# Kernel tuning notes

Measured on AMD Instinct MI355X. Metric: run time of the kernel, lower is better.

The kernel has to match this reference:

```python
import jax, jax.numpy as jnp
import numpy as np

DIM = 1024
ATT_DIM = 1024
NUM_HEADS = 16
HEAD_DIM = ATT_DIM // NUM_HEADS


def setup_inputs() -> dict:
    key = jax.random.key(0)
    ks = jax.random.split(key, 13)
    s = lambda fan_in: 1.0 / np.sqrt(fan_in)
    bsz, n = 8, 1024
    x = jax.random.normal(ks[0], (bsz, n, DIM), dtype=jnp.float32)
    # Linear weights stored as [in, out] (apply via x @ W + b)
    Wq = jax.random.uniform(ks[1], (DIM, ATT_DIM), minval=-s(DIM), maxval=s(DIM))
    bq = jax.random.uniform(ks[2], (ATT_DIM,), minval=-s(DIM), maxval=s(DIM))
    Wk = jax.random.uniform(ks[3], (DIM, ATT_DIM), minval=-s(DIM), maxval=s(DIM))
    bk = jax.random.uniform(ks[4], (ATT_DIM,), minval=-s(DIM), maxval=s(DIM))
    Wv = jax.random.uniform(ks[5], (DIM, ATT_DIM), minval=-s(DIM), maxval=s(DIM))
    bv = jax.random.uniform(ks[6], (ATT_DIM,), minval=-s(DIM), maxval=s(DIM))
    Win = jax.random.uniform(ks[7], (DIM, HEAD_DIM), minval=-s(DIM), maxval=s(DIM))
    bin_ = jax.random.uniform(ks[8], (HEAD_DIM,), minval=-s(DIM), maxval=s(DIM))
    d_in1 = HEAD_DIM * (NUM_HEADS + 1)
    W1 = jax.random.uniform(ks[9], (d_in1, 2 * DIM), minval=-s(d_in1), maxval=s(d_in1))
    b1 = jax.random.uniform(ks[10], (2 * DIM,), minval=-s(d_in1), maxval=s(d_in1))
    W2 = jax.random.uniform(ks[11], (2 * DIM, DIM), minval=-s(2 * DIM), maxval=s(2 * DIM))
    b2 = jax.random.uniform(ks[12], (DIM,), minval=-s(2 * DIM), maxval=s(2 * DIM))
    return {"x": x, "Wq": Wq, "bq": bq, "Wk": Wk, "bk": bk, "Wv": Wv, "bv": bv,
            "Win": Win, "bin_": bin_, "W1": W1, "b1": b1, "W2": W2, "b2": b2}


def reference(x, Wq, bq, Wk, bk, Wv, bv, Win, bin_, W1, b1, W2, b2):
    bsz, n, _ = x.shape
    scaling = HEAD_DIM ** (-0.5)
    # [b, n, h, d]
    q = (x @ Wq + bq).reshape(bsz, n, NUM_HEADS, HEAD_DIM) * scaling
    k = (x @ Wk + bk).reshape(bsz, n, NUM_HEADS, HEAD_DIM)
    v = (x @ Wv + bv).reshape(bsz, n, NUM_HEADS, HEAD_DIM)
    # scores [b, h, n, n]
    score = jnp.einsum('bihd,bjhd->bhij', q, k)
    diag = jnp.eye(n, dtype=bool)  # self positions masked with -inf
    score = jnp.where(diag[None, None], -jnp.inf, score)
    attn = jax.nn.softmax(score, axis=-1)
    out = jnp.einsum('bhij,bjhd->bihd', attn, v).reshape(bsz, n, NUM_HEADS * HEAD_DIM)
    in_ = (x @ Win + bin_)  # [b, n, head_dim]
    out = jnp.concatenate([out, in_], axis=-1)
    h = jax.nn.relu(out @ W1 + b1)
    return h @ W2 + b2
```

## Files before the change

kernel.cpp:

```cpp
#include <hip/hip_runtime.h>

typedef __bf16 bf16;
typedef __attribute__((ext_vector_type(8))) __bf16 bf16x8;
typedef __attribute__((ext_vector_type(4))) __bf16 bf16x4;
typedef __attribute__((ext_vector_type(4))) short short4_t;
typedef __attribute__((ext_vector_type(4))) float floatx4;

typedef const void __attribute__((address_space(1)))* gas1p;
typedef void __attribute__((address_space(3)))* las3p;

#define LOG2E 1.44269504088896340736f

static constexpr int D_MODEL = 1024;
static constexpr int N_HEADS = 16;
static constexpr int HDIM    = 64;
static constexpr int BSZ     = 8;
static constexpr int SEQ     = 1024;
static constexpr int ROWS    = BSZ * SEQ;
static constexpr int FF_IN   = 1088;
static constexpr int FF_HID  = 2048;
static constexpr int QKV_LD  = 3072;

__device__ __forceinline__ floatx4 mfma_bf16(bf16x8 a, bf16x8 b, floatx4 c) {
  return __builtin_amdgcn_mfma_f32_16x16x32_bf16(a, b, c, 0, 0, 0);
}

__device__ __forceinline__ floatx4 mfma16(bf16x4 a, bf16x4 b, floatx4 c) {
#if __has_builtin(__builtin_amdgcn_mfma_f32_16x16x16_bf16)
  return __builtin_amdgcn_mfma_f32_16x16x16_bf16(a, b, c, 0, 0, 0);
#else
  return __builtin_amdgcn_mfma_f32_16x16x16bf16_1k(
      __builtin_bit_cast(short4_t, a), __builtin_bit_cast(short4_t, b), c, 0, 0, 0);
#endif
}

__device__ __forceinline__ float flex_load(const void* src, size_t idx, int isbf) {
  return isbf ? (float)((const bf16*)src)[idx] : ((const float*)src)[idx];
}

__global__ void detect_kernel(const unsigned* __restrict__ w, int* __restrict__ flag) {
  __shared__ int cnt;
  if (threadIdx.x == 0) cnt = 0;
  __syncthreads();
  int hits = 0;
  for (int i = threadIdx.x; i < 4096; i += 256) {
    const unsigned v = w[(size_t)i * 997 + 13];
    const unsigned b = (v >> 8) & 0x7F;
    hits += (b >= 0x3B && b <= 0x41) ? 1 : 0;
  }
  atomicAdd(&cnt, hits);
  __syncthreads();
  if (threadIdx.x == 0) *flag = (cnt > 2048) ? 1 : 0;
}

__global__ __launch_bounds__(256)
void x_to_bf16_kernel(const void* __restrict__ src, bf16* __restrict__ dst,
                      const int* __restrict__ flag) {
  const int isbf = *flag;
  const size_t i = ((size_t)blockIdx.x * 256 + threadIdx.x) * 8;
  bf16x8 o;
  if (isbf) {
    o = *reinterpret_cast<const bf16x8*>((const bf16*)src + i);
  } else {
    const float4 f0 = *reinterpret_cast<const float4*>((const float*)src + i);
    const float4 f1 = *reinterpret_cast<const float4*>((const float*)src + i + 4);
    o[0] = (bf16)f0.x; o[1] = (bf16)f0.y; o[2] = (bf16)f0.z; o[3] = (bf16)f0.w;
    o[4] = (bf16)f1.x; o[5] = (bf16)f1.y; o[6] = (bf16)f1.z; o[7] = (bf16)f1.w;
  }
  *reinterpret_cast<bf16x8*>(dst + i) = o;
}

__global__ __launch_bounds__(256)
void bias_all_kernel(const void* bq, const void* bk, const void* bv,
                     const void* bin, const void* b1, const void* b2,
                     float* __restrict__ dst, const int* __restrict__ flag) {
  const int isbf = *flag;
  const int i = blockIdx.x * 256 + threadIdx.x;
  if (i < 1024)      dst[i] = flex_load(bq, i, isbf) * 0.125f;
  else if (i < 2048) dst[i] = flex_load(bk, i - 1024, isbf);
  else if (i < 3072) dst[i] = flex_load(bv, i - 2048, isbf);
  else if (i < 3136) dst[i] = flex_load(bin, i - 3072, isbf);
  else if (i < 5184) dst[i] = flex_load(b1, i - 3136, isbf);
  else if (i < 6208) dst[i] = flex_load(b2, i - 5184, isbf);
}

struct TransJobs {
  const void* src[6];
  bf16* dst[6];
  int R[6], C[6];
  int tiles_x[6];
  int tile_base[7];
  float scale[6];
};

__global__ __launch_bounds__(256)
void transpose_all_kernel(TransJobs J, const int* __restrict__ flag) {
  __shared__ float tile[32][33];
  const int isbf = *flag;
  const int bid = blockIdx.x;
  int j = 0;
#pragma unroll
  for (int t = 1; t < 6; t++) j += (bid >= J.tile_base[t]) ? 1 : 0;
  const int t = bid - J.tile_base[j];
  const int c0 = (t % J.tiles_x[j]) * 32, r0 = (t / J.tiles_x[j]) * 32;
  const void* src = J.src[j];
  bf16* dst = J.dst[j];
  const int R = J.R[j], C = J.C[j];
  const float scale = J.scale[j];
  const int tx = threadIdx.x & 31, ty = threadIdx.x >> 5;
  for (int i = ty; i < 32; i += 8)
    tile[i][tx] = flex_load(src, (size_t)(r0 + i) * C + (c0 + tx), isbf);
  __syncthreads();
  for (int i = ty; i < 32; i += 8)
    dst[(size_t)(c0 + i) * R + (r0 + tx)] = (bf16)(tile[tx][i] * scale);
}

__global__ __launch_bounds__(256)
void transpose_v_kernel(const bf16* __restrict__ v, bf16* __restrict__ vt) {
  __shared__ float tile[32][33];
  const int bh = blockIdx.z, b = bh >> 4, h = bh & 15;
  const int s0 = blockIdx.x * 32, d0 = blockIdx.y * 32;
  const int tx = threadIdx.x & 31, ty = threadIdx.x >> 5;
  const bf16* src = v + (size_t)b * SEQ * QKV_LD + 2048 + h * HDIM;
  bf16* dst = vt + (size_t)bh * HDIM * SEQ;
  for (int i = ty; i < 32; i += 8)
    tile[i][tx] = (float)src[(size_t)(s0 + i) * QKV_LD + d0 + tx];
  __syncthreads();
  for (int i = ty; i < 32; i += 8)
    dst[(size_t)(d0 + i) * SEQ + s0 + tx] = (bf16)tile[tx][i];
}

template <int BN, bool DO_RELU, bool OUT_FLEX>
__global__ __launch_bounds__(256)
void gemm_bt(const bf16* __restrict__ A, const bf16* __restrict__ BT,
             const float* __restrict__ bias,
             void* __restrict__ Cv, int N, int K, int ldc,
             bf16* __restrict__ C2, int ldc2, int nsplit, int nvalid,
             const int* __restrict__ flag) {
  constexpr int BM = 128, BK = 64;
  constexpr int TCN = BN / 32;
  constexpr int ACH = (BM * BK) / (256 * 8);
  constexpr int BCH = (BN * BK) / (256 * 8);
  __shared__ bf16 As[BM * BK];
  __shared__ bf16 Bs[BN * BK];
  const int tid = threadIdx.x;
  const int wave = tid >> 6, lane = tid & 63;
  const int quad = lane >> 4, lo = lane & 15;
  const int wm = wave >> 1, wn = wave & 1;
  const int m0 = blockIdx.x * BM;
  const int n0 = blockIdx.y * BN;

  floatx4 acc[4][TCN];
#pragma unroll
  for (int i = 0; i < 4; i++)
#pragma unroll
    for (int j = 0; j < TCN; j++) acc[i][j] = floatx4{0.f, 0.f, 0.f, 0.f};

  for (int kb = 0; kb < K; kb += BK) {
#pragma unroll
    for (int u = 0; u < ACH; u++) {
      const int c = u * 256 + tid;
      const int row = c >> 3, col = c & 7;
      const int gcol = col ^ (row & 7);
      const bf16* g = A + (size_t)(m0 + row) * K + kb + gcol * 8;
      __builtin_amdgcn_global_load_lds((gas1p)g, (las3p)(As + c * 8), 16, 0, 0);
    }
#pragma unroll
    for (int u = 0; u < BCH; u++) {
      const int c = u * 256 + tid;
      const int row = c >> 3, col = c & 7;
      const int gcol = col ^ (row & 7);
      const bf16* g = BT + (size_t)(n0 + row) * K + kb + gcol * 8;
      __builtin_amdgcn_global_load_lds((gas1p)g, (las3p)(Bs + c * 8), 16, 0, 0);
    }
    __syncthreads();
#pragma unroll
    for (int kk = 0; kk < 2; kk++) {
      bf16x8 af[4], bfr[TCN];
#pragma unroll
      for (int tr = 0; tr < 4; tr++) {
        const int row = wm * 64 + tr * 16 + lo;
        const int cc = (kk * 4 + quad) ^ (lo & 7);
        af[tr] = *reinterpret_cast<const bf16x8*>(As + row * BK + cc * 8);
      }
#pragma unroll
      for (int tc = 0; tc < TCN; tc++) {
        const int row = wn * (BN / 2) + tc * 16 + lo;
        const int cc = (kk * 4 + quad) ^ (lo & 7);
        bfr[tc] = *reinterpret_cast<const bf16x8*>(Bs + row * BK + cc * 8);
      }
#pragma unroll
      for (int tr = 0; tr < 4; tr++)
#pragma unroll
        for (int tc = 0; tc < TCN; tc++)
          acc[tr][tc] = mfma_bf16(af[tr], bfr[tc], acc[tr][tc]);
    }
    __syncthreads();
  }

  const int isbf = OUT_FLEX ? *flag : 1;
#pragma unroll
  for (int tc = 0; tc < TCN; tc++) {
    const int col = n0 + wn * (BN / 2) + tc * 16 + lo;
    const float bval = bias[col];
    if (col < nsplit) {
#pragma unroll
      for (int tr = 0; tr < 4; tr++) {
        const int rbase = m0 + wm * 64 + tr * 16 + quad * 4;
#pragma unroll
        for (int r = 0; r < 4; r++) {
          float v = acc[tr][tc][r] + bval;
          if (DO_RELU) v = fmaxf(v, 0.f);
          const size_t idx = (size_t)(rbase + r) * ldc + col;
          if (!OUT_FLEX || isbf) ((bf16*)Cv)[idx] = (bf16)v;
          else                   ((float*)Cv)[idx] = v;
        }
      }
    } else if (col < nvalid) {
#pragma unroll
      for (int tr = 0; tr < 4; tr++) {
        const int rbase = m0 + wm * 64 + tr * 16 + quad * 4;
#pragma unroll
        for (int r = 0; r < 4; r++) {
          float v = acc[tr][tc][r] + bval;
          if (DO_RELU) v = fmaxf(v, 0.f);
          C2[(size_t)(rbase + r) * ldc2 + (col - nsplit)] = (bf16)v;
        }
      }
    }
  }
}

__global__ __launch_bounds__(256)
void attn_kernel(const bf16* __restrict__ QKV, const bf16* __restrict__ Vt,
                 bf16* __restrict__ Cc) {
  __shared__ bf16 Ks[64 * 64];
  __shared__ bf16 Vs[64 * 64];
  const int bid = blockIdx.x;
  const int xcd = bid & 7, g = bid >> 3;
  const int ib = g & 7, bh = (g >> 3) * 8 + xcd;
  const int b = bh >> 4, h = bh & 15;
  const int i0 = ib * 128;
  const int tid = threadIdx.x, wave = tid >> 6, lane = tid & 63;
  const int quad = lane >> 4, lo = lane & 15;
  const int iw = i0 + wave * 32;
  const bf16* qptr = QKV + (size_t)b * SEQ * QKV_LD + h * HDIM;
  const bf16* kptr = QKV + (size_t)b * SEQ * QKV_LD + 1024 + h * HDIM;
  const bf16* vptr = Vt + (size_t)bh * HDIM * SEQ;

  bf16x8 qf[2][2];
#pragma unroll
  for (int it = 0; it < 2; it++)
#pragma unroll
    for (int kf = 0; kf < 2; kf++)
      qf[it][kf] = *reinterpret_cast<const bf16x8*>(
          qptr + (size_t)(iw + it * 16 + lo) * QKV_LD + kf * 32 + quad * 8);

  floatx4 oacc[2][4];
  float lrow[2] = {0.f, 0.f};
#pragma unroll
  for (int it = 0; it < 2; it++)
#pragma unroll
    for (int dt = 0; dt < 4; dt++) oacc[it][dt] = floatx4{0.f, 0.f, 0.f, 0.f};

  for (int jb = 0; jb < SEQ / 64; jb++) {
    const int j0 = jb * 64;
#pragma unroll
    for (int u = 0; u < 2; u++) {
      const int c = u * 256 + tid;
      const int row = c >> 3, col = c & 7;
      const int gcol = col ^ (row & 7);
      __builtin_amdgcn_global_load_lds(
          (gas1p)(kptr + (size_t)(j0 + row) * QKV_LD + gcol * 8),
          (las3p)(Ks + c * 8), 16, 0, 0);
      __builtin_amdgcn_global_load_lds(
          (gas1p)(vptr + (size_t)row * SEQ + j0 + gcol * 8),
          (las3p)(Vs + c * 8), 16, 0, 0);
    }
    __syncthreads();

    floatx4 sacc[2][4];
#pragma unroll
    for (int it = 0; it < 2; it++)
#pragma unroll
      for (int mt = 0; mt < 4; mt++) sacc[it][mt] = floatx4{0.f, 0.f, 0.f, 0.f};
#pragma unroll
    for (int mt = 0; mt < 4; mt++) {
      const int r = mt * 16 + lo;
      const int cc0 = quad ^ (lo & 7);
      const int cc1 = (4 + quad) ^ (lo & 7);
      const bf16x8 k0 = *reinterpret_cast<const bf16x8*>(Ks + r * 64 + cc0 * 8);
      const bf16x8 k1 = *reinterpret_cast<const bf16x8*>(Ks + r * 64 + cc1 * 8);
#pragma unroll
      for (int it = 0; it < 2; it++) {
        sacc[it][mt] = mfma_bf16(k0, qf[it][0], sacc[it][mt]);
        sacc[it][mt] = mfma_bf16(k1, qf[it][1], sacc[it][mt]);
      }
    }

    if (j0 == (iw & ~63)) {
#pragma unroll
      for (int it = 0; it < 2; it++) {
        const int ig = iw + it * 16 + lo;
#pragma unroll
        for (int mt = 0; mt < 4; mt++)
#pragma unroll
          for (int r = 0; r < 4; r++)
            if (j0 + mt * 16 + quad * 4 + r == ig) sacc[it][mt][r] = -1e30f;
      }
    }

    bf16x4 pfrag[2][4];
#pragma unroll
    for (int it = 0; it < 2; it++) {
      float s = 0.f;
#pragma unroll
      for (int mt = 0; mt < 4; mt++) {
        bf16x4 pk;
#pragma unroll
        for (int r = 0; r < 4; r++) {
          const float p = exp2f(sacc[it][mt][r] * LOG2E);
          s += p;
          pk[r] = (bf16)p;
        }
        pfrag[it][mt] = pk;
      }
      s += __shfl_xor(s, 16);
      s += __shfl_xor(s, 32);
      lrow[it] += s;
    }

#pragma unroll
    for (int dt = 0; dt < 4; dt++) {
      const int r = dt * 16 + lo;
#pragma unroll
      for (int kt = 0; kt < 4; kt++) {
        const int gch = kt * 2 + (quad >> 1);
        const int cc = gch ^ (lo & 7);
        const bf16x4 vf = *reinterpret_cast<const bf16x4*>(
            Vs + r * 64 + cc * 8 + (quad & 1) * 4);
#pragma unroll
        for (int it = 0; it < 2; it++)
          oacc[it][dt] = mfma16(vf, pfrag[it][kt], oacc[it][dt]);
      }
    }
    __syncthreads();
  }

#pragma unroll
  for (int it = 0; it < 2; it++) {
    const int ig = iw + it * 16 + lo;
    const float inv = 1.0f / lrow[it];
    bf16* cb = Cc + ((size_t)b * SEQ + ig) * FF_IN + h * HDIM;
#pragma unroll
    for (int dt = 0; dt < 4; dt++) {
      bf16x4 o;
#pragma unroll
      for (int r = 0; r < 4; r++) o[r] = (bf16)(oacc[it][dt][r] * inv);
      *reinterpret_cast<bf16x4*>(cb + dt * 16 + quad * 4) = o;
    }
  }
}

extern "C" void kernel_launch(void* const* d_in, const int* in_sizes, int n_in,
                              void* d_out, int out_size, void* d_ws, size_t ws_size,
                              hipStream_t stream) {
  (void)in_sizes; (void)n_in; (void)out_size; (void)ws_size;
  const void* x   = d_in[0];
  const void* Wq  = d_in[1];
  const void* bq  = d_in[2];
  const void* Wk  = d_in[3];
  const void* bk  = d_in[4];
  const void* Wv  = d_in[5];
  const void* bv  = d_in[6];
  const void* Win = d_in[7];
  const void* bin = d_in[8];
  const void* W1  = d_in[9];
  const void* b1  = d_in[10];
  const void* W2  = d_in[11];
  const void* b2  = d_in[12];

  size_t off = 0;
  char* wsb = (char*)d_ws;
  auto alloc = [&](size_t bytes) {
    void* p = (void*)(wsb + off);
    off += (bytes + 255) & ~(size_t)255;
    return p;
  };
  int*   flag  = (int*)alloc(4);
  bf16*  xbf   = (bf16*)alloc((size_t)ROWS * D_MODEL * 2);
  bf16*  WqkvT = (bf16*)alloc((size_t)3200 * 1024 * 2);
  bf16*  W1T   = (bf16*)alloc((size_t)FF_HID * FF_IN * 2);
  bf16*  W2T   = (bf16*)alloc((size_t)D_MODEL * FF_HID * 2);
  float* biasf = (float*)alloc(6208 * 4);
  bf16*  qkv   = (bf16*)alloc((size_t)ROWS * QKV_LD * 2);
  bf16*  vtb   = (bf16*)alloc((size_t)ROWS * D_MODEL * 2);
  bf16*  cbuf  = (bf16*)alloc((size_t)ROWS * FF_IN * 2);
  bf16*  hbuf  = (bf16*)alloc((size_t)ROWS * FF_HID * 2);
  float* b1f   = biasf + 3136;
  float* b2f   = biasf + 5184;

  const dim3 blk(256);
  detect_kernel<<<1, blk, 0, stream>>>((const unsigned*)x, flag);

  x_to_bf16_kernel<<<(ROWS * D_MODEL) / 2048, blk, 0, stream>>>(x, xbf, flag);
  bias_all_kernel<<<25, blk, 0, stream>>>(bq, bk, bv, bin, b1, b2, biasf, flag);

  TransJobs J;
  J.src[0] = Wq;  J.dst[0] = WqkvT;                        J.R[0] = 1024; J.C[0] = 1024; J.scale[0] = 0.125f;
  J.src[1] = Wk;  J.dst[1] = WqkvT + (size_t)1024 * 1024;  J.R[1] = 1024; J.C[1] = 1024; J.scale[1] = 1.0f;
  J.src[2] = Wv;  J.dst[2] = WqkvT + (size_t)2048 * 1024;  J.R[2] = 1024; J.C[2] = 1024; J.scale[2] = 1.0f;
  J.src[3] = Win; J.dst[3] = WqkvT + (size_t)3072 * 1024;  J.R[3] = 1024; J.C[3] = 64;   J.scale[3] = 1.0f;
  J.src[4] = W1;  J.dst[4] = W1T;                          J.R[4] = 1088; J.C[4] = 2048; J.scale[4] = 1.0f;
  J.src[5] = W2;  J.dst[5] = W2T;                          J.R[5] = 2048; J.C[5] = 1024; J.scale[5] = 1.0f;
  int base = 0;
  for (int j = 0; j < 6; j++) {
    J.tiles_x[j] = J.C[j] / 32;
    J.tile_base[j] = base;
    base += (J.R[j] / 32) * (J.C[j] / 32);
  }
  J.tile_base[6] = base;
  transpose_all_kernel<<<base, blk, 0, stream>>>(J, flag);

  gemm_bt<128, false, false><<<dim3(ROWS / 128, 25), blk, 0, stream>>>(
      xbf, WqkvT, biasf, qkv, 3200, 1024, QKV_LD,
      cbuf + 1024, FF_IN, 3072, 3136, nullptr);

  transpose_v_kernel<<<dim3(SEQ / 32, HDIM / 32, BSZ * N_HEADS), blk, 0, stream>>>(qkv, vtb);

  attn_kernel<<<dim3(1024), blk, 0, stream>>>(qkv, vtb, cbuf);

  gemm_bt<128, true, false><<<dim3(ROWS / 128, FF_HID / 128), blk, 0, stream>>>(
      cbuf, W1T, b1f, hbuf, FF_HID, FF_IN, FF_HID,
      nullptr, 0, FF_HID, FF_HID, nullptr);
  gemm_bt<128, false, true><<<dim3(ROWS / 128, D_MODEL / 128), blk, 0, stream>>>(
      hbuf, W2T, b2f, d_out, D_MODEL, FF_HID, D_MODEL,
      nullptr, 0, D_MODEL, D_MODEL, flag);
}
```

Baseline: 411.4 us.

## Fuse V transpose into QKV GEMM epilogue and shrink GEMM K-tile

The QKV projection GEMM now writes V directly in transposed per-head layout through an LDS staging tile in its epilogue. This removes the separate transpose_v kernel and the round trip of V through global memory, and the Q/K buffer shrinks to a 2048-wide stride. The GEMM K-tile is also reduced from 64 to 32 and the XOR swizzle is dropped. That halves LDS per block but doubles the number of barriers per K step and may bring back LDS bank conflicts in every GEMM.

After: 446.3 us. +8.5%, slower.

```diff
diff --git a/kernel.cpp b/kernel.cpp
--- a/kernel.cpp
+++ b/kernel.cpp
@@ -19,7 +19,7 @@
 static constexpr int ROWS    = BSZ * SEQ;
 static constexpr int FF_IN   = 1088;
 static constexpr int FF_HID  = 2048;
-static constexpr int QKV_LD  = 3072;
+static constexpr int QK_LD   = 2048;
 
 __device__ __forceinline__ floatx4 mfma_bf16(bf16x8 a, bf16x8 b, floatx4 c) {
   return __builtin_amdgcn_mfma_f32_16x16x32_bf16(a, b, c, 0, 0, 0);
@@ -115,34 +115,23 @@
     dst[(size_t)(c0 + i) * R + (r0 + tx)] = (bf16)(tile[tx][i] * scale);
 }
 
-__global__ __launch_bounds__(256)
-void transpose_v_kernel(const bf16* __restrict__ v, bf16* __restrict__ vt) {
-  __shared__ float tile[32][33];
-  const int bh = blockIdx.z, b = bh >> 4, h = bh & 15;
-  const int s0 = blockIdx.x * 32, d0 = blockIdx.y * 32;
-  const int tx = threadIdx.x & 31, ty = threadIdx.x >> 5;
-  const bf16* src = v + (size_t)b * SEQ * QKV_LD + 2048 + h * HDIM;
-  bf16* dst = vt + (size_t)bh * HDIM * SEQ;
-  for (int i = ty; i < 32; i += 8)
-    tile[i][tx] = (float)src[(size_t)(s0 + i) * QKV_LD + d0 + tx];
-  __syncthreads();
-  for (int i = ty; i < 32; i += 8)
-    dst[(size_t)(d0 + i) * SEQ + s0 + tx] = (bf16)tile[tx][i];
-}
-
-template <int BN, bool DO_RELU, bool OUT_FLEX>
+template <int BN, bool DO_RELU, bool OUT_FLEX, bool VTRANS>
 __global__ __launch_bounds__(256)
 void gemm_bt(const bf16* __restrict__ A, const bf16* __restrict__ BT,
              const float* __restrict__ bias,
              void* __restrict__ Cv, int N, int K, int ldc,
-             bf16* __restrict__ C2, int ldc2, int nsplit, int nvalid,
-             const int* __restrict__ flag) {
-  constexpr int BM = 128, BK = 64;
+             bf16* __restrict__ C2, int ldc2, int c2lo, int c2hi, int nsplit,
+             bf16* __restrict__ vtb, const int* __restrict__ flag) {
+  constexpr int BM = 128, BK = 32;
   constexpr int TCN = BN / 32;
   constexpr int ACH = (BM * BK) / (256 * 8);
   constexpr int BCH = (BN * BK) / (256 * 8);
-  __shared__ bf16 As[BM * BK];
-  __shared__ bf16 Bs[BN * BK];
+  constexpr int LDS_GEMM = (BM + BN) * BK * 2;
+  constexpr int LDS_VT   = 64 * 136 * 2;
+  constexpr int LDS_SZ   = (VTRANS && LDS_VT > LDS_GEMM) ? LDS_VT : LDS_GEMM;
+  __shared__ char lds_raw[LDS_SZ];
+  bf16* As = (bf16*)lds_raw;
+  bf16* Bs = As + BM * BK;
   const int tid = threadIdx.x;
   const int wave = tid >> 6, lane = tid & 63;
   const int quad = lane >> 4, lo = lane & 15;
@@ -160,42 +149,63 @@
 #pragma unroll
     for (int u = 0; u < ACH; u++) {
       const int c = u * 256 + tid;
-      const int row = c >> 3, col = c & 7;
-      const int gcol = col ^ (row & 7);
-      const bf16* g = A + (size_t)(m0 + row) * K + kb + gcol * 8;
+      const int row = c >> 2, cc = c & 3;
+      const bf16* g = A + (size_t)(m0 + row) * K + kb + cc * 8;
       __builtin_amdgcn_global_load_lds((gas1p)g, (las3p)(As + c * 8), 16, 0, 0);
     }
 #pragma unroll
     for (int u = 0; u < BCH; u++) {
       const int c = u * 256 + tid;
-      const int row = c >> 3, col = c & 7;
-      const int gcol = col ^ (row & 7);
-      const bf16* g = BT + (size_t)(n0 + row) * K + kb + gcol * 8;
+      const int row = c >> 2, cc = c & 3;
+      const bf16* g = BT + (size_t)(n0 + row) * K + kb + cc * 8;
       __builtin_amdgcn_global_load_lds((gas1p)g, (las3p)(Bs + c * 8), 16, 0, 0);
     }
     __syncthreads();
-#pragma unroll
-    for (int kk = 0; kk < 2; kk++) {
-      bf16x8 af[4], bfr[TCN];
-#pragma unroll
-      for (int tr = 0; tr < 4; tr++) {
-        const int row = wm * 64 + tr * 16 + lo;
-        const int cc = (kk * 4 + quad) ^ (lo & 7);
-        af[tr] = *reinterpret_cast<const bf16x8*>(As + row * BK + cc * 8);
-      }
-#pragma unroll
-      for (int tc = 0; tc < TCN; tc++) {
-        const int row = wn * (BN / 2) + tc * 16 + lo;
-        const int cc = (kk * 4 + quad) ^ (lo & 7);
-        bfr[tc] = *reinterpret_cast<const bf16x8*>(Bs + row * BK + cc * 8);
-      }
-#pragma unroll
-      for (int tr = 0; tr < 4; tr++)
-#pragma unroll
-        for (int tc = 0; tc < TCN; tc++)
-          acc[tr][tc] = mfma_bf16(af[tr], bfr[tc], acc[tr][tc]);
-    }
+    bf16x8 af[4], bfr[TCN];
+#pragma unroll
+    for (int tr = 0; tr < 4; tr++)
+      af[tr] = *reinterpret_cast<const bf16x8*>(As + (wm * 64 + tr * 16 + lo) * BK + quad * 8);
+#pragma unroll
+    for (int tc = 0; tc < TCN; tc++)
+      bfr[tc] = *reinterpret_cast<const bf16x8*>(Bs + (wn * (BN / 2) + tc * 16 + lo) * BK + quad * 8);
+#pragma unroll
+    for (int tr = 0; tr < 4; tr++)
+#pragma unroll
+      for (int tc = 0; tc < TCN; tc++)
+        acc[tr][tc] = mfma_bf16(af[tr], bfr[tc], acc[tr][tc]);
     __syncthreads();
+  }
+
+  if (VTRANS && n0 >= 2048 && n0 < 3072) {
+    const int bb = m0 >> 10, i0m = m0 & 1023;
+    bf16* vt_ls = (bf16*)lds_raw;
+#pragma unroll
+    for (int p = 0; p < 2; p++) {
+      if (wn == p) {
+#pragma unroll
+        for (int tc = 0; tc < TCN; tc++) {
+          const int d = tc * 16 + lo;
+          const float bval = bias[n0 + p * 64 + d];
+#pragma unroll
+          for (int tr = 0; tr < 4; tr++)
+#pragma unroll
+            for (int r = 0; r < 4; r++)
+              vt_ls[d * 136 + wm * 64 + tr * 16 + quad * 4 + r] =
+                  (bf16)(acc[tr][tc][r] + bval);
+        }
+      }
+      __syncthreads();
+      const int hh = (n0 + p * 64 - 2048) >> 6;
+      bf16* vbase = vtb + ((size_t)(bb * 16 + hh) * 64) * SEQ + i0m;
+      const int d = tid >> 2, iq = (tid & 3) * 32;
+#pragma unroll
+      for (int k = 0; k < 4; k++) {
+        const bf16x8 vv = *reinterpret_cast<const bf16x8*>(vt_ls + d * 136 + iq + k * 8);
+        *reinterpret_cast<bf16x8*>(vbase + (size_t)d * SEQ + iq + k * 8) = vv;
+      }
+      __syncthreads();
+    }
+    return;
   }
 
   const int isbf = OUT_FLEX ? *flag : 1;
@@ -216,7 +226,7 @@
           else                   ((float*)Cv)[idx] = v;
         }
       }
-    } else if (col < nvalid) {
+    } else if (col >= c2lo && col < c2hi) {
 #pragma unroll
       for (int tr = 0; tr < 4; tr++) {
         const int rbase = m0 + wm * 64 + tr * 16 + quad * 4;
@@ -224,7 +234,7 @@
         for (int r = 0; r < 4; r++) {
           float v = acc[tr][tc][r] + bval;
           if (DO_RELU) v = fmaxf(v, 0.f);
-          C2[(size_t)(rbase + r) * ldc2 + (col - nsplit)] = (bf16)v;
+          C2[(size_t)(rbase + r) * ldc2 + (col - c2lo)] = (bf16)v;
         }
       }
     }
@@ -232,7 +242,7 @@
 }
 
 __global__ __launch_bounds__(256)
-void attn_kernel(const bf16* __restrict__ QKV, const bf16* __restrict__ Vt,
+void attn_kernel(const bf16* __restrict__ QK, const bf16* __restrict__ Vt,
                  bf16* __restrict__ Cc) {
   __shared__ bf16 Ks[64 * 64];
   __shared__ bf16 Vs[64 * 64];
@@ -244,8 +254,8 @@
   const int tid = threadIdx.x, wave = tid >> 6, lane = tid & 63;
   const int quad = lane >> 4, lo = lane & 15;
   const int iw = i0 + wave * 32;
-  const bf16* qptr = QKV + (size_t)b * SEQ * QKV_LD + h * HDIM;
-  const bf16* kptr = QKV + (size_t)b * SEQ * QKV_LD + 1024 + h * HDIM;
+  const bf16* qptr = QK + (size_t)b * SEQ * QK_LD + h * HDIM;
+  const bf16* kptr = QK + (size_t)b * SEQ * QK_LD + 1024 + h * HDIM;
   const bf16* vptr = Vt + (size_t)bh * HDIM * SEQ;
 
   bf16x8 qf[2][2];
@@ -254,7 +264,7 @@
 #pragma unroll
     for (int kf = 0; kf < 2; kf++)
       qf[it][kf] = *reinterpret_cast<const bf16x8*>(
-          qptr + (size_t)(iw + it * 16 + lo) * QKV_LD + kf * 32 + quad * 8);
+          qptr + (size_t)(iw + it * 16 + lo) * QK_LD + kf * 32 + quad * 8);
 
   floatx4 oacc[2][4];
   float lrow[2] = {0.f, 0.f};
@@ -271,7 +281,7 @@
       const int row = c >> 3, col = c & 7;
       const int gcol = col ^ (row & 7);
       __builtin_amdgcn_global_load_lds(
-          (gas1p)(kptr + (size_t)(j0 + row) * QKV_LD + gcol * 8),
+          (gas1p)(kptr + (size_t)(j0 + row) * QK_LD + gcol * 8),
           (las3p)(Ks + c * 8), 16, 0, 0);
       __builtin_amdgcn_global_load_lds(
           (gas1p)(vptr + (size_t)row * SEQ + j0 + gcol * 8),
@@ -393,7 +403,7 @@
   bf16*  W1T   = (bf16*)alloc((size_t)FF_HID * FF_IN * 2);
   bf16*  W2T   = (bf16*)alloc((size_t)D_MODEL * FF_HID * 2);
   float* biasf = (float*)alloc(6208 * 4);
-  bf16*  qkv   = (bf16*)alloc((size_t)ROWS * QKV_LD * 2);
+  bf16*  qk    = (bf16*)alloc((size_t)ROWS * QK_LD * 2);
   bf16*  vtb   = (bf16*)alloc((size_t)ROWS * D_MODEL * 2);
   bf16*  cbuf  = (bf16*)alloc((size_t)ROWS * FF_IN * 2);
   bf16*  hbuf  = (bf16*)alloc((size_t)ROWS * FF_HID * 2);
@@ -422,18 +432,16 @@
   J.tile_base[6] = base;
   transpose_all_kernel<<<base, blk, 0, stream>>>(J, flag);
 
-  gemm_bt<128, false, false><<<dim3(ROWS / 128, 25), blk, 0, stream>>>(
-      xbf, WqkvT, biasf, qkv, 3200, 1024, QKV_LD,
-      cbuf + 1024, FF_IN, 3072, 3136, nullptr);
-
-  transpose_v_kernel<<<dim3(SEQ / 32, HDIM / 32, BSZ * N_HEADS), blk, 0, stream>>>(qkv, vtb);
-
-  attn_kernel<<<dim3(1024), blk, 0, stream>>>(qkv, vtb, cbuf);
-
-  gemm_bt<128, true, false><<<dim3(ROWS / 128, FF_HID / 128), blk, 0, stream>>>(
+  gemm_bt<128, false, false, true><<<dim3(ROWS / 128, 25), blk, 0, stream>>>(
+      xbf, WqkvT, biasf, qk, 3200, 1024, QK_LD,
+      cbuf + 1024, FF_IN, 3072, 3136, 2048, vtb, nullptr);
+
+  attn_kernel<<<dim3(1024), blk, 0, stream>>>(qk, vtb, cbuf);
+
+  gemm_bt<128, true, false, false><<<dim3(ROWS / 128, FF_HID / 128), blk, 0, stream>>>(
       cbuf, W1T, b1f, hbuf, FF_HID, FF_IN, FF_HID,
-      nullptr, 0, FF_HID, FF_HID, nullptr);
-  gemm_bt<128, false, true><<<dim3(ROWS / 128, D_MODEL / 128), blk, 0, stream>>>(
+      nullptr, 0, FF_HID, FF_HID, FF_HID, nullptr, nullptr);
+  gemm_bt<128, false, true, false><<<dim3(ROWS / 128, D_MODEL / 128), blk, 0, stream>>>(
       hbuf, W2T, b2f, d_out, D_MODEL, FF_HID, D_MODEL,
-      nullptr, 0, D_MODEL, D_MODEL, flag);
-}
+      nullptr, 0, D_MODEL, D_MODEL, D_MODEL, nullptr, flag);
+}
```
